# Performance work log

Hardware: AMD Instinct MI355X
Metric: run time of the kernel (lower is better)

Reference implementation:

```python
import jax, jax.numpy as jnp
import numpy as np

N_STEPS = 20
ALPHA, BETA = 0.9, 0.8  # synaptic / membrane decay (unused given zero carried state, kept for clarity)


def _lcn_spiking_layer(h, knn, w, b):
    """h: [N, d_in]; knn: [d_out, K] indices into d_in; w: [d_out, K]; b: [1, d_out].
    Gather K neighbors per output node, weight, reduce, then snntorch Synaptic
    update with zero carried state (the source never stores returned syn/mem):
      syn = ALPHA*0 + I = I ; reset = (prev_mem > thr) = 0 ; mem = BETA*0 + syn - 0 = I
    and the layer output is mem (the source keeps the 3rd return value)."""
    g = h[:, knn]                                  # [N, d_out, K] irregular gather
    cur = jnp.sum(g * w[None, :, :], axis=2) + b   # [N, d_out]
    syn = ALPHA * jnp.zeros_like(cur) + cur
    mem = BETA * jnp.zeros_like(cur) + syn         # reset term is zero
    return mem


def setup_inputs() -> dict:
    key = jax.random.key(0)
    B, T, IN_DIM, K, OUT = 32, N_STEPS, 14400, 25, 2
    dims = [7200, 3600, 1800, 900, 450]
    ks = jax.random.split(key, 13)
    inp = {"x": jax.random.normal(ks[0], (B, T, IN_DIM), dtype=jnp.float32)}
    prev = IN_DIM
    for i, d in enumerate(dims):
        inp[f"w{i}"] = jax.random.normal(ks[1 + i], (d, K), dtype=jnp.float32) * (2.0 / K) ** 0.5
        inp[f"b{i}"] = jnp.zeros((1, d), dtype=jnp.float32)
        inp[f"knn{i}"] = jax.random.randint(ks[6 + i], (d, K), 0, prev)
        prev = d
    inp["Wfc"] = jax.random.normal(ks[11], (dims[-1], OUT), dtype=jnp.float32) * (1.0 / dims[-1]) ** 0.5
    inp["bfc"] = jnp.zeros((OUT,), dtype=jnp.float32)
    return inp


def reference(x, w0, w1, w2, w3, w4, b0, b1, b2, b3, b4, Wfc, bfc,
              knn0, knn1, knn2, knn3, knn4):
    # Source loops over 20 timesteps with independent (state never carried) work;
    # fold time into batch to vectorize, then keep the last step's angle only,
    # exactly matching the returned value of the torch forward.
    B, T, D = x.shape
    h = x.reshape(B * T, D)
    layers = ((w0, b0, knn0), (w1, b1, knn1), (w2, b2, knn2), (w3, b3, knn3), (w4, b4, knn4))
    for w, b, knn in layers:
        h = _lcn_spiking_layer(h, knn, w, b)
    angle = h @ Wfc + bfc                     # [B*T, out_dim]
    angle = angle.reshape(B, T, -1)[:, -1]    # last timestep, as in the source
    return angle
```

## Files before the change

kernel.cpp:

```cpp
#include <hip/hip_runtime.h>


#define ROWS 32
#define TSTEPS 20
#define D0 14400
#define D1 7200
#define D2 3600
#define D3 1800
#define D4 900
#define D5 450
#define KNB 25

__global__ __launch_bounds__(256)
void l0_stage(const float* __restrict__ x, float* __restrict__ h1t,
              const float* __restrict__ w, const float* __restrict__ bvec,
              const int* __restrict__ knn)
{
    __shared__ float s[D0];
    const int r = blockIdx.y;
    const float* xrow = x + ((size_t)r * TSTEPS + (TSTEPS - 1)) * (size_t)D0;

    const float4* src = reinterpret_cast<const float4*>(xrow);
    float4* dst = reinterpret_cast<float4*>(s);
#pragma unroll 1
    for (int i = threadIdx.x; i < D0 / 4; i += 256)
        dst[i] = src[i];
    __syncthreads();

    const int j0 = blockIdx.x * 900;
#pragma unroll 1
    for (int j = j0 + threadIdx.x; j < j0 + 900; j += 256) {
        const int*   kn = knn + j * KNB;
        const float* ww = w   + j * KNB;
        float acc = bvec[j];
#pragma unroll
        for (int k = 0; k < KNB; ++k)
            acc += s[kn[k]] * ww[k];
        h1t[(j << 5) + r] = acc;
    }
}

__global__ __launch_bounds__(256)
void layer_t_k(const float* __restrict__ pin, float* __restrict__ pout,
               const float* __restrict__ w, const float* __restrict__ bvec,
               const int* __restrict__ knn, int npairs)
{
    const int lane = threadIdx.x & 63;
    const int r  = lane & 31;
    const int jj = lane >> 5;
    const int nw = gridDim.x << 2;
#pragma unroll 1
    for (int jp = (blockIdx.x << 2) + (threadIdx.x >> 6); jp < npairs; jp += nw) {
        const int j = (jp << 1) + jj;
        const int*   kn = knn + j * KNB;
        const float* ww = w   + j * KNB;
        float acc = bvec[j];
#pragma unroll
        for (int k = 0; k < KNB; ++k)
            acc += pin[(kn[k] << 5) + r] * ww[k];
        pout[(j << 5) + r] = acc;
    }
}

__global__ __launch_bounds__(512)
void tail_fused(const float* __restrict__ h2t,
                const float* __restrict__ w2, const float* __restrict__ b2, const int* __restrict__ n2,
                const float* __restrict__ w3, const float* __restrict__ b3, const int* __restrict__ n3,
                const float* __restrict__ w4, const float* __restrict__ b4, const int* __restrict__ n4,
                const float* __restrict__ Wfc, const float* __restrict__ bfc,
                float* __restrict__ out)
{
    __shared__ float s2[D2];
    __shared__ float s3[D3];
    __shared__ float s4[D4];
    __shared__ float s5[D5];
    __shared__ float red[2];

    const int r   = blockIdx.x;
    const int tid = threadIdx.x;

#pragma unroll 1
    for (int j = tid; j < D2; j += 512)
        s2[j] = h2t[(j << 5) + r];
    __syncthreads();

#pragma unroll 1
    for (int j = tid; j < D3; j += 512) {
        const int*   kn = n2 + j * KNB;
        const float* ww = w2 + j * KNB;
        float acc = b2[j];
#pragma unroll
        for (int k = 0; k < KNB; ++k)
            acc += s2[kn[k]] * ww[k];
        s3[j] = acc;
    }
    __syncthreads();

#pragma unroll 1
    for (int j = tid; j < D4; j += 512) {
        const int*   kn = n3 + j * KNB;
        const float* ww = w3 + j * KNB;
        float acc = b3[j];
#pragma unroll
        for (int k = 0; k < KNB; ++k)
            acc += s3[kn[k]] * ww[k];
        s4[j] = acc;
    }
    __syncthreads();

#pragma unroll 1
    for (int j = tid; j < D5; j += 512) {
        const int*   kn = n4 + j * KNB;
        const float* ww = w4 + j * KNB;
        float acc = b4[j];
#pragma unroll
        for (int k = 0; k < KNB; ++k)
            acc += s4[kn[k]] * ww[k];
        s5[j] = acc;
    }

    if (tid == 0) { red[0] = bfc[0]; red[1] = bfc[1]; }
    __syncthreads();

    float c0 = 0.0f, c1 = 0.0f;
    if (tid < D5) {
        const float v = s5[tid];
        c0 = v * Wfc[2 * tid + 0];
        c1 = v * Wfc[2 * tid + 1];
    }
#pragma unroll
    for (int off = 32; off > 0; off >>= 1) {
        c0 += __shfl_down(c0, off);
        c1 += __shfl_down(c1, off);
    }
    if ((tid & 63) == 0) {
        atomicAdd(&red[0], c0);
        atomicAdd(&red[1], c1);
    }
    __syncthreads();
    if (tid < 2)
        out[2 * r + tid] = red[tid];
}

extern "C" void kernel_launch(void* const* d_in, const int* in_sizes, int n_in,
                              void* d_out, int out_size, void* d_ws, size_t ws_size,
                              hipStream_t stream)
{
    const float* x    = (const float*)d_in[0];
    const float* w0   = (const float*)d_in[1];
    const float* b0   = (const float*)d_in[2];
    const int*   knn0 = (const int*)  d_in[3];
    const float* w1   = (const float*)d_in[4];
    const float* b1   = (const float*)d_in[5];
    const int*   knn1 = (const int*)  d_in[6];
    const float* w2   = (const float*)d_in[7];
    const float* b2   = (const float*)d_in[8];
    const int*   knn2 = (const int*)  d_in[9];
    const float* w3   = (const float*)d_in[10];
    const float* b3   = (const float*)d_in[11];
    const int*   knn3 = (const int*)  d_in[12];
    const float* w4   = (const float*)d_in[13];
    const float* b4   = (const float*)d_in[14];
    const int*   knn4 = (const int*)  d_in[15];
    const float* Wfc  = (const float*)d_in[16];
    const float* bfc  = (const float*)d_in[17];
    float* out = (float*)d_out;

    float* h1t = (float*)d_ws;
    float* h2t = h1t + (size_t)D1 * ROWS;

    l0_stage<<<dim3(D1 / 900, ROWS), dim3(256), 0, stream>>>(x, h1t, w0, b0, knn0);

    layer_t_k<<<dim3(450), dim3(256), 0, stream>>>(h1t, h2t, w1, b1, knn1, D2 / 2);

    tail_fused<<<dim3(ROWS), dim3(512), 0, stream>>>(
        h2t,
        w2, b2, knn2,
        w3, b3, knn3,
        w4, b4, knn4,
        Wfc, bfc, out);
}
```

Baseline: 134.0 us.

## Split layer 2 out of tail kernel into grid-wide row-major gather kernel

Layer 2 (3600->1800) moves out of the 32-block tail kernel into its own kernel with 225 blocks. That kernel writes its output row-major so the tail can copy it with float4 loads. The aim is to spread layer-2 work across many more CUs, since the old tail kernel ran only 32 blocks and did a strided transposing load of h2t. In exchange it adds a kernel launch and a global round trip for the layer-3 input, and the row-major stores are strided across lanes.

```diff
diff --git a/kernel.cpp b/kernel.cpp
--- a/kernel.cpp
+++ b/kernel.cpp
@@ -62,15 +62,35 @@
     }
 }
 
+__global__ __launch_bounds__(256)
+void layer_t_k_rm(const float* __restrict__ pin, float* __restrict__ pout,
+                  const float* __restrict__ w, const float* __restrict__ bvec,
+                  const int* __restrict__ knn, int npairs, int dout)
+{
+    const int lane = threadIdx.x & 63;
+    const int r  = lane & 31;
+    const int jj = lane >> 5;
+    const int nw = gridDim.x << 2;
+#pragma unroll 1
+    for (int jp = (blockIdx.x << 2) + (threadIdx.x >> 6); jp < npairs; jp += nw) {
+        const int j = (jp << 1) + jj;
+        const int*   kn = knn + j * KNB;
+        const float* ww = w   + j * KNB;
+        float acc = bvec[j];
+#pragma unroll
+        for (int k = 0; k < KNB; ++k)
+            acc += pin[(kn[k] << 5) + r] * ww[k];
+        pout[r * dout + j] = acc;
+    }
+}
+
 __global__ __launch_bounds__(512)
-void tail_fused(const float* __restrict__ h2t,
-                const float* __restrict__ w2, const float* __restrict__ b2, const int* __restrict__ n2,
-                const float* __restrict__ w3, const float* __restrict__ b3, const int* __restrict__ n3,
-                const float* __restrict__ w4, const float* __restrict__ b4, const int* __restrict__ n4,
-                const float* __restrict__ Wfc, const float* __restrict__ bfc,
-                float* __restrict__ out)
+void tail34fc(const float* __restrict__ h3,
+              const float* __restrict__ w3, const float* __restrict__ b3, const int* __restrict__ n3,
+              const float* __restrict__ w4, const float* __restrict__ b4, const int* __restrict__ n4,
+              const float* __restrict__ Wfc, const float* __restrict__ bfc,
+              float* __restrict__ out)
 {
-    __shared__ float s2[D2];
     __shared__ float s3[D3];
     __shared__ float s4[D4];
     __shared__ float s5[D5];
@@ -79,20 +99,12 @@
     const int r   = blockIdx.x;
     const int tid = threadIdx.x;
 
+    {
+        const float4* src = reinterpret_cast<const float4*>(h3 + (size_t)r * D3);
+        float4* dst = reinterpret_cast<float4*>(s3);
 #pragma unroll 1
-    for (int j = tid; j < D2; j += 512)
-        s2[j] = h2t[(j << 5) + r];
-    __syncthreads();
-
-#pragma unroll 1
-    for (int j = tid; j < D3; j += 512) {
-        const int*   kn = n2 + j * KNB;
-        const float* ww = w2 + j * KNB;
-        float acc = b2[j];
-#pragma unroll
-        for (int k = 0; k < KNB; ++k)
-            acc += s2[kn[k]] * ww[k];
-        s3[j] = acc;
+        for (int i = tid; i < D3 / 4; i += 512)
+            dst[i] = src[i];
     }
     __syncthreads();
 
@@ -168,14 +180,16 @@
 
     float* h1t = (float*)d_ws;
     float* h2t = h1t + (size_t)D1 * ROWS;
+    float* h3  = h2t + (size_t)D2 * ROWS;
 
     l0_stage<<<dim3(D1 / 900, ROWS), dim3(256), 0, stream>>>(x, h1t, w0, b0, knn0);
 
     layer_t_k<<<dim3(450), dim3(256), 0, stream>>>(h1t, h2t, w1, b1, knn1, D2 / 2);
 
-    tail_fused<<<dim3(ROWS), dim3(512), 0, stream>>>(
-        h2t,
-        w2, b2, knn2,
+    layer_t_k_rm<<<dim3(225), dim3(256), 0, stream>>>(h2t, h3, w2, b2, knn2, D3 / 2, D3);
+
+    tail34fc<<<dim3(ROWS), dim3(512), 0, stream>>>(
+        h3,
         w3, b3, knn3,
         w4, b4, knn4,
         Wfc, bfc, out);
```

New measurement: 129.6 us. 1.03x faster.
